# Kernel optimization log

Measured on AMD Instinct MI355X. Metric: run time of the kernel, lower is better.

The kernel has to match this reference:

```python
import jax, jax.numpy as jnp
import numpy as np

B, L, D, H, P = 8, 1024, 128, 128, 8
W = 2 * L  # total words
FT = 0.1   # forget-gate floor


def _lin_init(k, out_d, in_d):
    k1, k2 = jax.random.split(k)
    s = 1.0 / np.sqrt(in_d)
    Wm = jax.random.uniform(k1, (out_d, in_d), minval=-s, maxval=s, dtype=jnp.float32)
    b = jax.random.uniform(k2, (out_d,), minval=-s, maxval=s, dtype=jnp.float32)
    return Wm, b


def setup_inputs() -> dict:
    key = jax.random.key(0)
    ks = jax.random.split(key, 32)
    inp = {
        "word_span0": jax.random.normal(ks[0], (B, L, D), dtype=jnp.float32),
        "word_span1": jax.random.normal(ks[1], (B, L, D), dtype=jnp.float32),
        "node_hidden": jax.random.normal(ks[2], (B, D), dtype=jnp.float32),
        "op_embedding": jax.random.normal(ks[3], (B, P, D), dtype=jnp.float32),
        "word_exist_sequence": jax.random.uniform(ks[4], (B, W), dtype=jnp.float32),
        "word_exist_matrix": jax.random.uniform(ks[5], (B, W, W), dtype=jnp.float32),
        "word_operator": jax.random.uniform(ks[6], (B, W, P), dtype=jnp.float32),
        "word_word": jax.random.uniform(ks[7], (B, W, W), dtype=jnp.float32),
        "depend0": jax.random.uniform(ks[8], (B, L, L), dtype=jnp.float32),
        "depend1": jax.random.uniform(ks[9], (B, L, L), dtype=jnp.float32),
        "goal_word": jax.random.uniform(ks[10], (B, W), dtype=jnp.float32),
    }
    dims = [("w_w_s", H, D), ("w_w_k", H, D), ("w_update", D, 3 * H),
            ("g_w", H, D), ("w_o", D, D), ("b2u_forget", D, 3 * H + D),
            ("b2u_forget2", D, 2 * D), ("linear_output", D, D),
            ("o_w", H, D), ("w_g", D, D), ("u2b_forget", D, 2 * D),
            ("w_o_forget", P, D + P * D), ("w_o_rel", P, D + P * D),
            ("w_o_update", P, 2 * P)]
    for i, (nm, o, ii) in enumerate(dims):
        Wm, b = _lin_init(ks[11 + i], o, ii)
        inp[nm + "_W"] = Wm
        inp[nm + "_b"] = b
    return inp


def _lin(x, Wm, b):
    return x @ Wm.T + b


def _nrm(m):
    # row-normalize by count of nonzero entries (torch normalize_matrix)
    return m / ((m != 0).sum(-1, keepdims=True).astype(m.dtype) + 1e-30)


def _l2(x):
    return x / (jnp.linalg.norm(x, axis=-1, keepdims=True) + 1e-30)


def _hgcn(span0, span1, node_hidden, op_emb, wes, wem, w_op, ww, dep0, dep1, gw, p):
    # ---- Bottom2Up ----
    all_word = jnp.concatenate([span0, span1], axis=1)              # [B,W,D]
    goal_trans = _lin(node_hidden, p["g_w_W"], p["g_w_b"])[:, None, :]  # [B,1,H]
    word_g = _l2(goal_trans * gw[..., None])                        # [B,W,H]
    wk_trans = _lin(all_word, p["w_w_k_W"], p["w_w_k_b"])           # [B,W,H]
    word_w_k = _l2(_nrm(ww * wem) @ wk_trans)                       # [B,W,H]
    word_w_s = _l2(jnp.concatenate(
        [_nrm(dep0) @ _lin(span0, p["w_w_s_W"], p["w_w_s_b"]),
         _nrm(dep1) @ _lin(span1, p["w_w_s_W"], p["w_w_s_b"])], axis=1))
    neighbor = jnp.concatenate([word_g, word_w_k, word_w_s], axis=-1)  # [B,W,3H]
    forget = jax.nn.sigmoid(_lin(jnp.concatenate([all_word, word_g, word_w_k, word_w_s], axis=-1),
                                 p["b2u_forget_W"], p["b2u_forget_b"]))
    word_updated = jnp.clip(forget, FT) * all_word + (1 - forget) * jax.nn.relu(
        _lin(neighbor, p["w_update_W"], p["w_update_b"]))           # [B,W,D]
    word_op = _nrm(jnp.swapaxes(wes[..., None] * w_op, 1, 2)) @ _lin(
        word_updated, p["w_o_W"], p["w_o_b"])                       # [B,P,D]
    forget2 = jax.nn.sigmoid(_lin(jnp.concatenate([op_emb, word_op], axis=-1),
                                  p["b2u_forget2_W"], p["b2u_forget2_b"]))
    op_emb = jnp.clip(forget2, FT) * op_emb + (1 - forget2) * jax.nn.relu(
        _lin(word_op, p["linear_output_W"], p["linear_output_b"]))  # [B,P,D]

    # ---- update_graph ----
    awe_n = _l2(word_updated)
    op_n = _l2(op_emb).reshape(op_emb.shape[0], -1)                 # [B,P*D]
    concate = jnp.concatenate(
        [awe_n, jnp.broadcast_to(op_n[:, None, :], (awe_n.shape[0], awe_n.shape[1], op_n.shape[-1]))],
        axis=-1)                                                    # [B,W,D+P*D]
    fg = jnp.clip(jax.nn.sigmoid(_lin(concate, p["w_o_forget_W"], p["w_o_forget_b"])), FT)
    upd = jax.nn.softmax(jax.nn.relu(_lin(
        jnp.concatenate([w_op, _lin(concate, p["w_o_rel_W"], p["w_o_rel_b"])], axis=-1),
        p["w_o_update_W"], p["w_o_update_b"])), axis=-1)
    w_op_new = fg * w_op + (1 - fg) * upd                           # [B,W,P]

    # ---- Up2Bottom ----
    span0u, span1u = word_updated[:, :L], word_updated[:, L:]
    word_o = _l2(w_op_new @ _lin(op_emb, p["o_w_W"], p["o_w_b"]))   # [B,W,H]
    word_w_k2 = _l2(_nrm(ww * wem) @ _lin(word_updated, p["w_w_k_W"], p["w_w_k_b"]))
    word_w_s2 = _l2(jnp.concatenate(
        [_nrm(dep0) @ _lin(span0u, p["w_w_s_W"], p["w_w_s_b"]),
         _nrm(dep1) @ _lin(span1u, p["w_w_s_W"], p["w_w_s_b"])], axis=1))
    neighbor2 = jnp.concatenate([word_o, word_w_k2, word_w_s2], axis=-1)
    word_updated2 = jax.nn.relu(_lin(neighbor2, p["w_update_W"], p["w_update_b"]))  # [B,W,D]
    goal_w = jnp.einsum('bw,bwd->bd', _nrm(gw * wes), word_updated2)  # [B,D]
    goal_updated = jax.nn.relu(_lin(goal_w, p["w_g_W"], p["w_g_b"]))
    fg3 = jax.nn.sigmoid(_lin(jnp.concatenate([goal_w, node_hidden], axis=-1),
                              p["u2b_forget_W"], p["u2b_forget_b"]))
    goal_next = jnp.clip(fg3, FT) * node_hidden + (1 - fg3) * goal_updated
    return (span0u, span1u, op_emb, goal_next)


def reference(word_span0, word_span1, node_hidden, op_embedding, word_exist_sequence,
              word_exist_matrix, word_operator, word_word, depend0, depend1, goal_word,
              w_w_s_W, w_w_s_b, w_w_k_W, w_w_k_b, w_update_W, w_update_b,
              g_w_W, g_w_b, w_o_W, w_o_b, b2u_forget_W, b2u_forget_b,
              b2u_forget2_W, b2u_forget2_b, linear_output_W, linear_output_b,
              o_w_W, o_w_b, w_g_W, w_g_b, u2b_forget_W, u2b_forget_b,
              w_o_forget_W, w_o_forget_b, w_o_rel_W, w_o_rel_b, w_o_update_W, w_o_update_b):
    p = dict(w_w_s_W=w_w_s_W, w_w_s_b=w_w_s_b, w_w_k_W=w_w_k_W, w_w_k_b=w_w_k_b,
             w_update_W=w_update_W, w_update_b=w_update_b, g_w_W=g_w_W, g_w_b=g_w_b,
             w_o_W=w_o_W, w_o_b=w_o_b, b2u_forget_W=b2u_forget_W, b2u_forget_b=b2u_forget_b,
             b2u_forget2_W=b2u_forget2_W, b2u_forget2_b=b2u_forget2_b,
             linear_output_W=linear_output_W, linear_output_b=linear_output_b,
             o_w_W=o_w_W, o_w_b=o_w_b, w_g_W=w_g_W, w_g_b=w_g_b,
             u2b_forget_W=u2b_forget_W, u2b_forget_b=u2b_forget_b,
             w_o_forget_W=w_o_forget_W, w_o_forget_b=w_o_forget_b,
             w_o_rel_W=w_o_rel_W, w_o_rel_b=w_o_rel_b,
             w_o_update_W=w_o_update_W, w_o_update_b=w_o_update_b)
    return _hgcn(word_span0, word_span1, node_hidden, op_embedding, word_exist_sequence,
                 word_exist_matrix, word_operator, word_word, depend0, depend1, goal_word, p)
```

## Files before the change

### kernel.cpp

```cpp
#include <hip/hip_runtime.h>

constexpr int Bn = 8, Ln = 1024, Dn = 128, Pn = 8, Wn = 2048;
constexpr float FTc = 0.1f;
constexpr int BLDc = Bn * Ln * Dn;
constexpr int BWDc = Bn * Wn * Dn;
constexpr int IDM = 1 << 28;

struct __align__(16) F4 { float v[4]; };

typedef __attribute__((ext_vector_type(8))) __bf16 bf16x8;
typedef __attribute__((ext_vector_type(8))) short short8v;
typedef __attribute__((ext_vector_type(4))) short short4v;
typedef __attribute__((ext_vector_type(4))) float f32x4;

static __device__ __forceinline__ float sigm(float x) { return 1.f / (1.f + expf(-x)); }

static __device__ __forceinline__ short f2bf(float f) {
    unsigned u = __builtin_bit_cast(unsigned, f);
    unsigned r = (u + 0x7FFFu + ((u >> 16) & 1u)) >> 16;
    return (short)r;
}

template<int NSRC, int ACT, int OUT, int BM>
__global__ __launch_bounds__(256)
void linmfma(const short* __restrict__ x0, const short* __restrict__ x1,
             const short* __restrict__ x2, const short* __restrict__ x3,
             const float* __restrict__ Wt, const float* __restrict__ bias,
             float* __restrict__ Y, short* __restrict__ Yh, short* __restrict__ Xblk,
             int in_mod, int in_stride, int in_off,
             int out_mod, int out_stride, int out_off,
             const float* __restrict__ fbuf, const float* __restrict__ bbuf)
{
    constexpr int K = NSRC * 128;
    constexpr int NKB = K / 64;
    constexpr int WRr = BM / 16;
    constexpr int WC = 4 / WRr;
    constexpr int NF = 8 / WC;
    constexpr int CPW = 128 / WC;
    __shared__ short sX[BM * 72];
    __shared__ short sW[128 * 72];

    const int tid = threadIdx.x;
    const int wave = tid >> 6, lane = tid & 63;
    const int l15 = lane & 15, l4 = lane >> 4;
    const int rg = wave % WRr, cg = wave / WRr;
    const int n0 = blockIdx.x * BM;
    const int inRow0  = (n0 / in_mod)  * in_stride  + (n0 % in_mod)  + in_off;
    const int outRow0 = (n0 / out_mod) * out_stride + (n0 % out_mod) + out_off;

    f32x4 acc[NF];
    #pragma unroll
    for (int nf = 0; nf < NF; ++nf) acc[nf] = (f32x4){0.f, 0.f, 0.f, 0.f};

    const int xrow = tid >> 3, xk8 = (tid & 7) * 8;

    for (int kb = 0; kb < NKB; ++kb) {
        const int k0 = kb * 64;
        __syncthreads();
        if (tid < BM * 8) {
            const short* __restrict__ src;
            { int s = k0 >> 7; src = (s == 0) ? x0 : (s == 1) ? x1 : (s == 2) ? x2 : x3; }
            const int koff = k0 & 127;
            *(short8v*)&sX[xrow * 72 + xk8] =
                *(const short8v*)(src + (size_t)(inRow0 + xrow) * 128 + koff + xk8);
        }
        #pragma unroll
        for (int it = 0; it < 4; ++it) {
            int idx = tid + it * 256;
            int m = idx >> 3, k8 = (idx & 7) * 8;
            const float* pw = Wt + (size_t)m * K + k0 + k8;
            F4 v0 = *(const F4*)pw, v1 = *(const F4*)(pw + 4);
            short8v sv;
            #pragma unroll
            for (int e = 0; e < 4; ++e) { sv[e] = f2bf(v0.v[e]); sv[4 + e] = f2bf(v1.v[e]); }
            *(short8v*)&sW[m * 72 + k8] = sv;
        }
        __syncthreads();
        #pragma unroll
        for (int ksub = 0; ksub < 2; ++ksub) {
            bf16x8 af = *(const bf16x8*)&sX[(rg * 16 + l15) * 72 + ksub * 32 + l4 * 8];
            #pragma unroll
            for (int nf = 0; nf < NF; ++nf) {
                bf16x8 bv = *(const bf16x8*)&sW[(cg * CPW + nf * 16 + l15) * 72 + ksub * 32 + l4 * 8];
                acc[nf] = __builtin_amdgcn_mfma_f32_16x16x32_bf16(af, bv, acc[nf], 0, 0, 0);
            }
        }
    }

    const int r0 = rg * 16 + l4 * 4;
    float vals[NF][4];
    #pragma unroll
    for (int nf = 0; nf < NF; ++nf) {
        int col = cg * CPW + nf * 16 + l15;
        float bs = bias[col];
        #pragma unroll
        for (int r = 0; r < 4; ++r) {
            int row = outRow0 + r0 + r;
            float v = acc[nf][r] + bs;
            if constexpr (ACT == 1) v = fmaxf(v, 0.f);
            if constexpr (ACT == 2) v = sigm(v);
            if constexpr (ACT == 3) {
                float f = fbuf[(size_t)row * 128 + col];
                float base = bbuf[(size_t)row * 128 + col];
                v = fmaxf(f, FTc) * base + (1.f - f) * fmaxf(v, 0.f);
            }
            vals[nf][r] = v;
            if constexpr (OUT & 1) Y[(size_t)row * 128 + col] = v;
            if constexpr (OUT & 2) Yh[(size_t)row * 128 + col] = f2bf(v);
        }
    }
    if constexpr (OUT & 4) {
        short* sS = sW;
        __syncthreads();
        #pragma unroll
        for (int nf = 0; nf < NF; ++nf) {
            int col = cg * CPW + nf * 16 + l15;
            #pragma unroll
            for (int r = 0; r < 4; ++r)
                sS[col * 40 + r0 + r] = f2bf(vals[nf][r]);
        }
        __syncthreads();
        const int bb = outRow0 >> 11, kbo = (outRow0 & 2047) >> 5;
        short* __restrict__ dst = Xblk + ((size_t)(bb * 64 + kbo)) * 4096;
        #pragma unroll
        for (int it = 0; it < 2; ++it) {
            int t2 = tid + it * 256;
            int col = t2 >> 2, k8 = (t2 & 3) * 8;
            *(short8v*)(dst + (size_t)t2 * 8) = *(const short8v*)&sS[col * 40 + k8];
        }
    }
}

template<int AMODE, bool WRA>
__global__ __launch_bounds__(256)
void mfma_part(const float* __restrict__ A0, const float* __restrict__ A1,
               const short* __restrict__ Abf, short* __restrict__ Awr,
               const short* __restrict__ Xblk, float* __restrict__ part,
               int NI, int KJ, int KL, int xkb0)
{
    __shared__ short sA[32 * 72];
    __shared__ short sB[128 * 72];
    const int tid = threadIdx.x;
    const int wave = tid >> 6, lane = tid & 63;
    const int l15 = lane & 15, l4 = lane >> 4;
    const int rg = wave >> 1, cg = wave & 1;
    const int b = blockIdx.y, kc = blockIdx.z;
    const int i0 = blockIdx.x * 32;
    const size_t aBase = ((size_t)b * NI + i0) * KJ + (size_t)kc * KL;
    const int nkb = KL >> 6;
    const int cbase = b * 64 + xkb0 + ((kc * KL) >> 5);
    const int arow = tid >> 3, ak16 = (tid & 7) * 8, ak8 = (tid & 3) * 8;

    f32x4 acc[4];
    #pragma unroll
    for (int nf = 0; nf < 4; ++nf) acc[nf] = (f32x4){0.f, 0.f, 0.f, 0.f};

    short8v ra;
    F4 rav0, rav1, raw0, raw1;
    short8v rb0, rb1, rb2, rb3;

#define LOADA(KB)                                                              \
    {                                                                          \
        size_t aoff = aBase + (size_t)arow * KJ + (KB)*64 + ak16;              \
        if constexpr (AMODE == 2) {                                            \
            ra = *(const short8v*)(Abf + aoff);                                \
        } else {                                                               \
            rav0 = *(const F4*)(A0 + aoff); rav1 = *(const F4*)(A0 + aoff + 4);\
            if constexpr (AMODE == 1) {                                        \
                raw0 = *(const F4*)(A1 + aoff); raw1 = *(const F4*)(A1 + aoff + 4); \
            }                                                                  \
        }                                                                      \
    }
#define STOREA(KB)                                                             \
    {                                                                          \
        short8v sv;                                                            \
        if constexpr (AMODE == 2) { sv = ra; }                                 \
        else {                                                                 \
            _Pragma("unroll")                                                  \
            for (int e = 0; e < 4; ++e) {                                      \
                float f0 = rav0.v[e], f1 = rav1.v[e];                          \
                if constexpr (AMODE == 1) { f0 *= raw0.v[e]; f1 *= raw1.v[e]; }\
                sv[e] = f2bf(f0); sv[4 + e] = f2bf(f1);                        \
            }                                                                  \
        }                                                                      \
        *(short8v*)&sA[arow * 72 + ak16] = sv;                                 \
        if constexpr (WRA)                                                     \
            *(short8v*)(Awr + aBase + (size_t)arow * KJ + (KB)*64 + ak16) = sv;\
    }
#define LOADB(KB)                                                              \
    {                                                                          \
        const short* s0 = Xblk + ((size_t)(cbase + (KB)*2)) * 4096;            \
        rb0 = *(const short8v*)(s0 + (size_t)tid * 8);                         \
        rb1 = *(const short8v*)(s0 + (size_t)(tid + 256) * 8);                 \
        rb2 = *(const short8v*)(s0 + 4096 + (size_t)tid * 8);                  \
        rb3 = *(const short8v*)(s0 + 4096 + (size_t)(tid + 256) * 8);          \
    }
#define STOREB()                                                               \
    {                                                                          \
        int c0 = tid >> 2;            int c1 = (tid + 256) >> 2;               \
        *(short8v*)&sB[c0 * 72 + ak8]      = rb0;                              \
        *(short8v*)&sB[c1 * 72 + ak8]      = rb1;                              \
        *(short8v*)&sB[c0 * 72 + 32 + ak8] = rb2;                              \
        *(short8v*)&sB[c1 * 72 + 32 + ak8] = rb3;                              \
    }

    LOADA(0); LOADB(0);
    STOREA(0); STOREB();
    __syncthreads();

    for (int kb = 0; kb < nkb; ++kb) {
        const bool more = (kb + 1 < nkb);
        if (more) { LOADA(kb + 1); LOADB(kb + 1); }
        #pragma unroll
        for (int ksub = 0; ksub < 2; ++ksub) {
            bf16x8 af = *(const bf16x8*)&sA[(rg * 16 + l15) * 72 + ksub * 32 + l4 * 8];
            #pragma unroll
            for (int nf = 0; nf < 4; ++nf) {
                bf16x8 bv = *(const bf16x8*)&sB[(cg * 64 + nf * 16 + l15) * 72 + ksub * 32 + l4 * 8];
                acc[nf] = __builtin_amdgcn_mfma_f32_16x16x32_bf16(af, bv, acc[nf], 0, 0, 0);
            }
        }
        if (more) {
            __syncthreads();
            STOREA(kb + 1); STOREB();
            __syncthreads();
        }
    }
#undef LOADA
#undef STOREA
#undef LOADB
#undef STOREB

    const size_t pbase = (((size_t)kc * Bn + b) * NI + i0 + rg * 16 + l4 * 4) * 128 + cg * 64;
    #pragma unroll
    for (int nf = 0; nf < 4; ++nf)
        #pragma unroll
        for (int r = 0; r < 4; ++r)
            part[pbase + (size_t)r * 128 + nf * 16 + l15] = acc[nf][r];
}

__global__ void k_gemm_fin(const float* __restrict__ part, short* __restrict__ Yh,
                           int NI, int KCH, int ybs, int yoff)
{
    int row = blockIdx.x; int b = row / NI; int i = row - b * NI;
    int h = threadIdx.x;
    float s = 0.f;
    for (int kc = 0; kc < KCH; ++kc)
        s += part[(((size_t)kc * Bn + b) * NI + i) * 128 + h];
    __shared__ float red[128];
    red[h] = s * s; __syncthreads();
    for (int st = 64; st > 0; st >>= 1) { if (h < st) red[h] += red[h + st]; __syncthreads(); }
    Yh[(size_t)(b * ybs + yoff + i) * 128 + h] = f2bf(s / (sqrtf(red[0]) + 1e-30f));
}

__global__ void k_allword(const float* __restrict__ s0, const float* __restrict__ s1,
                          float* __restrict__ aw, short* __restrict__ awh)
{
    int i = blockIdx.x * 256 + threadIdx.x;
    int b = i / (Ln * Dn / 4);
    F4 v0 = ((const F4*)s0)[i];
    F4 v1 = ((const F4*)s1)[i];
    int d0 = i + b * (Ln * Dn / 4);
    int d1 = i + (b + 1) * (Ln * Dn / 4);
    ((F4*)aw)[d0] = v0;
    ((F4*)aw)[d1] = v1;
    short4v h0, h1;
    #pragma unroll
    for (int e = 0; e < 4; ++e) { h0[e] = f2bf(v0.v[e]); h1[e] = f2bf(v1.v[e]); }
    ((short4v*)awh)[d0] = h0;
    ((short4v*)awh)[d1] = h1;
}

__global__ void k_goalg(const float* __restrict__ node, const float* __restrict__ Wg,
                        const float* __restrict__ bg, float* __restrict__ gvec,
                        float* __restrict__ gnorm)
{
    int b = blockIdx.x, h = threadIdx.x;
    float s = bg[h];
    for (int k = 0; k < 128; ++k) s += node[b * 128 + k] * Wg[h * 128 + k];
    gvec[b * 128 + h] = s;
    __shared__ float red[128];
    red[h] = s * s; __syncthreads();
    for (int st = 64; st > 0; st >>= 1) { if (h < st) red[h] += red[h + st]; __syncthreads(); }
    if (h == 0) gnorm[b] = sqrtf(red[0]);
}

__global__ void k_wordg(const float* __restrict__ gvec, const float* __restrict__ gnorm,
                        const float* __restrict__ gw, short* __restrict__ wgh)
{
    int row = blockIdx.x; int b = row >> 11; int h = threadIdx.x;
    float s = gw[row];
    float coef = s / (s * gnorm[b] + 1e-30f);
    wgh[(size_t)row * 128 + h] = f2bf(gvec[b * 128 + h] * coef);
}

__global__ __launch_bounds__(256)
void k_wordop_part(const float* __restrict__ wes, const float* __restrict__ wopr,
                   const float* __restrict__ Yl, float* __restrict__ part,
                   float* __restrict__ pcnt)
{
    int c = blockIdx.x, b = blockIdx.y;
    int w0 = c * 32;
    __shared__ float sc[32][8];
    int tid = threadIdx.x;
    {
        int w = tid >> 3, p = tid & 7;
        sc[w][p] = wes[b * Wn + w0 + w] * wopr[(size_t)(b * Wn + w0 + w) * Pn + p];
    }
    __syncthreads();
    if (tid < 8) {
        float n = 0.f;
        for (int w = 0; w < 32; ++w) n += (sc[w][tid] != 0.f) ? 1.f : 0.f;
        pcnt[(c * 8 + b) * 8 + tid] = n;
    }
    int d = tid & 127, g = tid >> 7;
    float acc[4] = {};
    for (int w = 0; w < 32; ++w) {
        float y = Yl[(size_t)(b * Wn + w0 + w) * 128 + d];
        #pragma unroll
        for (int q = 0; q < 4; ++q) acc[q] += sc[w][g * 4 + q] * y;
    }
    #pragma unroll
    for (int q = 0; q < 4; ++q)
        part[(((size_t)c * 8 + b) * 8 + g * 4 + q) * 128 + d] = acc[q];
}

__global__ void k_wordop_fin(const float* __restrict__ part, const float* __restrict__ pcnt,
                             float* __restrict__ outp)
{
    int bp = blockIdx.x;
    int b = bp >> 3, p = bp & 7;
    int d = threadIdx.x;
    float s = 0.f, n = 0.f;
    for (int c = 0; c < 64; ++c) s += part[(((size_t)c * 8 + b) * 8 + p) * 128 + d];
    for (int c = 0; c < 64; ++c) n += pcnt[(c * 8 + b) * 8 + p];
    outp[(size_t)bp * 128 + d] = s / (n + 1e-30f);
}

__global__ void k_opemb(const float* __restrict__ oein, const float* __restrict__ wop,
                        const float* __restrict__ W2, const float* __restrict__ b2,
                        const float* __restrict__ Wlo, const float* __restrict__ blo,
                        float* __restrict__ opembN, float* __restrict__ out2)
{
    int bp = blockIdx.x; int h = threadIdx.x;
    const float* oe = oein + (size_t)bp * 128;
    const float* wo = wop + (size_t)bp * 128;
    float s = b2[h], lo = blo[h];
    for (int k = 0; k < 128; ++k) {
        s += oe[k] * W2[h * 256 + k];
        s += wo[k] * W2[h * 256 + 128 + k];
        lo += wo[k] * Wlo[h * 128 + k];
    }
    float f = sigm(s);
    float v = fmaxf(f, FTc) * oe[h] + (1.f - f) * fmaxf(lo, 0.f);
    opembN[bp * 128 + h] = v;
    out2[bp * 128 + h] = v;
}

__global__ void k_opn(const float* __restrict__ opembN, float* __restrict__ opn)
{
    __shared__ float red[128];
    int bp = blockIdx.x, h = threadIdx.x;
    float v = opembN[bp * 128 + h];
    red[h] = v * v; __syncthreads();
    for (int s = 64; s > 0; s >>= 1) { if (h < s) red[h] += red[h + s]; __syncthreads(); }
    opn[bp * 128 + h] = v / (sqrtf(red[0]) + 1e-30f);
}

__global__ void k_cfrel(const float* __restrict__ opn, const float* __restrict__ Wf,
                        const float* __restrict__ bf, const float* __restrict__ Wr,
                        const float* __restrict__ br, float* __restrict__ cf,
                        float* __restrict__ crel)
{
    int bp = blockIdx.x; int b = bp >> 3, p = bp & 7;
    int t = threadIdx.x;
    float sf = 0.f, sr = 0.f;
    for (int k = t; k < 1024; k += 256) {
        float o = opn[b * 1024 + k];
        sf += o * Wf[p * 1152 + 128 + k];
        sr += o * Wr[p * 1152 + 128 + k];
    }
    __shared__ float rf[256], rr[256];
    rf[t] = sf; rr[t] = sr; __syncthreads();
    for (int s = 128; s > 0; s >>= 1) {
        if (t < s) { rf[t] += rf[t + s]; rr[t] += rr[t + s]; }
        __syncthreads();
    }
    if (t == 0) { cf[bp] = rf[0] + bf[p]; crel[bp] = rr[0] + br[p]; }
}

__global__ __launch_bounds__(256)
void k_fgrel(const float* __restrict__ wupd, const float* __restrict__ Wf,
             const float* __restrict__ Wr, const float* __restrict__ cf,
             const float* __restrict__ crel, float* __restrict__ fgb,
             float* __restrict__ relb)
{
    __shared__ float sXr[32 * 132];
    __shared__ float sinv[32];
    int tid = threadIdx.x;
    int n0 = blockIdx.x * 32;
    for (int l = tid; l < 4096; l += 256) {
        int r = l >> 7, h = l & 127;
        sXr[r * 132 + h] = wupd[(size_t)(n0 + r) * 128 + h];
    }
    __syncthreads();
    if (tid < 32) {
        float s = 0.f;
        for (int h = 0; h < 128; ++h) { float v = sXr[tid * 132 + h]; s += v * v; }
        sinv[tid] = 1.f / (sqrtf(s) + 1e-30f);
    }
    __syncthreads();
    int r = tid >> 3, p = tid & 7;
    int n = n0 + r; int b = n >> 11;
    float af = 0.f, ar = 0.f, inv = sinv[r];
    for (int d = 0; d < 128; ++d) {
        float x = sXr[r * 132 + d] * inv;
        af += x * Wf[p * 1152 + d];
        ar += x * Wr[p * 1152 + d];
    }
    float f = sigm(af + cf[b * 8 + p]);
    fgb[(size_t)n * 8 + p] = fmaxf(f, FTc);
    relb[(size_t)n * 8 + p] = ar + crel[b * 8 + p];
}

__global__ void k_wopnew(const float* __restrict__ wopr, const float* __restrict__ fgb,
                         const float* __restrict__ relb, const float* __restrict__ Wu,
                         const float* __restrict__ bu, float* __restrict__ wopn)
{
    int row = blockIdx.x * 256 + threadIdx.x;
    float t16[16];
    #pragma unroll
    for (int p = 0; p < 8; ++p) t16[p] = wopr[(size_t)row * 8 + p];
    #pragma unroll
    for (int p = 0; p < 8; ++p) t16[8 + p] = relb[(size_t)row * 8 + p];
    float u[8]; float m = -1e30f;
    #pragma unroll
    for (int p = 0; p < 8; ++p) {
        float s = bu[p];
        #pragma unroll
        for (int q = 0; q < 16; ++q) s += Wu[p * 16 + q] * t16[q];
        s = fmaxf(s, 0.f); u[p] = s; m = fmaxf(m, s);
    }
    float tot = 0.f;
    #pragma unroll
    for (int p = 0; p < 8; ++p) { u[p] = expf(u[p] - m); tot += u[p]; }
    float itot = 1.f / tot;
    #pragma unroll
    for (int p = 0; p < 8; ++p) {
        float f = fgb[(size_t)row * 8 + p];
        wopn[(size_t)row * 8 + p] = f * t16[p] + (1.f - f) * u[p] * itot;
    }
}

__global__ void k_opw(const float* __restrict__ opembN, const float* __restrict__ Wo,
                      const float* __restrict__ bo, float* __restrict__ opw)
{
    int bp = blockIdx.x, h = threadIdx.x;
    float s = bo[h];
    for (int d = 0; d < 128; ++d) s += opembN[bp * 128 + d] * Wo[h * 128 + d];
    opw[bp * 128 + h] = s;
}

__global__ void k_wordo(const float* __restrict__ wopn, const float* __restrict__ opw,
                        short* __restrict__ woh)
{
    int row = blockIdx.x; int b = row >> 11; int h = threadIdx.x;
    float c[8];
    #pragma unroll
    for (int p = 0; p < 8; ++p) c[p] = wopn[(size_t)row * 8 + p];
    float v = 0.f;
    #pragma unroll
    for (int p = 0; p < 8; ++p) v += c[p] * opw[(b * 8 + p) * 128 + h];
    __shared__ float red[128];
    red[h] = v * v; __syncthreads();
    for (int s = 64; s > 0; s >>= 1) { if (h < s) red[h] += red[h + s]; __syncthreads(); }
    woh[(size_t)row * 128 + h] = f2bf(v / (sqrtf(red[0]) + 1e-30f));
}

__global__ __launch_bounds__(256)
void k_goalw_part(const float* __restrict__ gw, const float* __restrict__ wes,
                  const float* __restrict__ wupd2, float* __restrict__ part,
                  float* __restrict__ pcnt)
{
    int c = blockIdx.x, b = blockIdx.y;
    int w0 = c * 32;
    __shared__ float sc[32];
    __shared__ float sa[256];
    int tid = threadIdx.x;
    if (tid < 32) sc[tid] = gw[b * Wn + w0 + tid] * wes[b * Wn + w0 + tid];
    __syncthreads();
    if (tid == 0) {
        float n = 0.f;
        for (int w = 0; w < 32; ++w) n += (sc[w] != 0.f) ? 1.f : 0.f;
        pcnt[c * 8 + b] = n;
    }
    int d = tid & 127, h = tid >> 7;
    float acc = 0.f;
    for (int w = h; w < 32; w += 2)
        acc += sc[w] * wupd2[(size_t)(b * Wn + w0 + w) * 128 + d];
    sa[tid] = acc; __syncthreads();
    if (h == 0) part[((size_t)c * 8 + b) * 128 + d] = sa[d] + sa[128 + d];
}

__global__ void k_goalw_fin(const float* __restrict__ part, const float* __restrict__ pcnt,
                            float* __restrict__ goalw)
{
    int b = blockIdx.x, d = threadIdx.x;
    float s = 0.f, n = 0.f;
    for (int c = 0; c < 64; ++c) s += part[((size_t)c * 8 + b) * 128 + d];
    for (int c = 0; c < 64; ++c) n += pcnt[c * 8 + b];
    goalw[b * 128 + d] = s / (n + 1e-30f);
}

__global__ void k_goalnext(const float* __restrict__ goalw, const float* __restrict__ node,
                           const float* __restrict__ Wg, const float* __restrict__ bg,
                           const float* __restrict__ Wu2, const float* __restrict__ bu2,
                           float* __restrict__ outg)
{
    int b = blockIdx.x, h = threadIdx.x;
    float su = bg[h], sf = bu2[h];
    for (int k = 0; k < 128; ++k) {
        float g = goalw[b * 128 + k];
        su += g * Wg[h * 128 + k];
        sf += g * Wu2[h * 256 + k] + node[b * 128 + k] * Wu2[h * 256 + 128 + k];
    }
    float gu = fmaxf(su, 0.f);
    float f = sigm(sf);
    outg[b * 128 + h] = fmaxf(f, FTc) * node[b * 128 + h] + (1.f - f) * gu;
}

__global__ void k_copyspans(const float* __restrict__ wupd, float* __restrict__ out)
{
    int i = blockIdx.x * 256 + threadIdx.x;
    F4 v = ((const F4*)wupd)[i];
    int row = i >> 5;
    int col = i & 31;
    int b = row >> 11, w = row & 2047;
    int dst;
    if (w < Ln) dst = ((b * Ln + w) << 5) + col;
    else        dst = (BLDc >> 2) + ((b * Ln + (w - Ln)) << 5) + col;
    ((F4*)out)[dst] = v;
}

extern "C" void kernel_launch(void* const* d_in, const int* in_sizes, int n_in,
                              void* d_out, int out_size, void* d_ws, size_t ws_size,
                              hipStream_t stream)
{
    const float* span0 = (const float*)d_in[0];
    const float* span1 = (const float*)d_in[1];
    const float* node  = (const float*)d_in[2];
    const float* opemb = (const float*)d_in[3];
    const float* wes   = (const float*)d_in[4];
    const float* wem   = (const float*)d_in[5];
    const float* wopr  = (const float*)d_in[6];
    const float* ww    = (const float*)d_in[7];
    const float* dep0  = (const float*)d_in[8];
    const float* dep1  = (const float*)d_in[9];
    const float* gw    = (const float*)d_in[10];
    const float* wws_W = (const float*)d_in[11]; const float* wws_b = (const float*)d_in[12];
    const float* wwk_W = (const float*)d_in[13]; const float* wwk_b = (const float*)d_in[14];
    const float* wup_W = (const float*)d_in[15]; const float* wup_b = (const float*)d_in[16];
    const float* gw_W  = (const float*)d_in[17]; const float* gw_b  = (const float*)d_in[18];
    const float* wo_W  = (const float*)d_in[19]; const float* wo_b  = (const float*)d_in[20];
    const float* bf_W  = (const float*)d_in[21]; const float* bf_b  = (const float*)d_in[22];
    const float* bf2_W = (const float*)d_in[23]; const float* bf2_b = (const float*)d_in[24];
    const float* lo_W  = (const float*)d_in[25]; const float* lo_b  = (const float*)d_in[26];
    const float* ow_W  = (const float*)d_in[27]; const float* ow_b  = (const float*)d_in[28];
    const float* wg_W  = (const float*)d_in[29]; const float* wg_b  = (const float*)d_in[30];
    const float* u2b_W = (const float*)d_in[31]; const float* u2b_b = (const float*)d_in[32];
    const float* wof_W = (const float*)d_in[33]; const float* wof_b = (const float*)d_in[34];
    const float* wor_W = (const float*)d_in[35]; const float* wor_b = (const float*)d_in[36];
    const float* wou_W = (const float*)d_in[37]; const float* wou_b = (const float*)d_in[38];

    float* out = (float*)d_out;
    float* out_op   = out + 2 * BLDc;
    float* out_goal = out + 2 * BLDc + Bn * Pn * Dn;

    float* ws = (float*)d_ws;
    float* allword = ws;
    float* wupd    = ws + 1 * BWDc;
    float* tmpA    = ws + 2 * BWDc;
    float* tmpB    = ws + 3 * BWDc;
    float* sm      = ws + 4 * BWDc;
    float* gvec   = sm;
    float* gnorm  = sm + 1024;
    float* wordop = sm + 1056;
    float* opembN = sm + 9248;
    float* opn    = sm + 17440;
    float* cf     = sm + 25632;
    float* crel   = sm + 25696;
    float* opw    = sm + 25760;
    float* goalw  = sm + 33952;
    float* fgb    = sm + 34976;
    float* relb   = sm + 166048;
    float* wopn   = sm + 297120;

    short* allwordh = (short*)(ws + 4 * (size_t)BWDc + 458752);
    short* wupdh  = allwordh + BWDc;
    short* wordgh = wupdh + BWDc;
    short* wwkh   = wordgh + BWDc;
    short* wwsh   = wwkh + BWDc;
    short* Xblk   = wwsh + BWDc;
    short* Awwem  = Xblk + BWDc;
    short* dep0b  = Awwem + (size_t)Bn * Wn * Wn;
    short* dep1b  = dep0b + (size_t)Bn * Ln * Ln;

    float* partWW1 = (float*)dep0b;
    float* partWW2 = tmpA;
    float* partD0  = tmpA;
    float* partD1  = tmpB;

    const dim3 blk(256);

    k_allword<<<1024, blk, 0, stream>>>(span0, span1, allword, allwordh);
    linmfma<1,0,4,32><<<512, blk, 0, stream>>>(allwordh, nullptr, nullptr, nullptr,
        wwk_W, wwk_b, nullptr, nullptr, Xblk, IDM, 0, 0, IDM, 0, 0, nullptr, nullptr);
    mfma_part<1,true><<<dim3(64, 8, 4), blk, 0, stream>>>(ww, wem, nullptr, Awwem,
        Xblk, partWW1, Wn, Wn, 512, 0);
    k_gemm_fin<<<16384, 128, 0, stream>>>(partWW1, wwkh, Wn, 4, Wn, 0);
    linmfma<1,0,4,32><<<256, blk, 0, stream>>>(allwordh, nullptr, nullptr, nullptr,
        wws_W, wws_b, nullptr, nullptr, Xblk, Ln, Wn, 0, Ln, Wn, 0, nullptr, nullptr);
    linmfma<1,0,4,32><<<256, blk, 0, stream>>>(allwordh, nullptr, nullptr, nullptr,
        wws_W, wws_b, nullptr, nullptr, Xblk, Ln, Wn, Ln, Ln, Wn, Ln, nullptr, nullptr);
    mfma_part<0,true><<<dim3(32, 8, 2), blk, 0, stream>>>(dep0, nullptr, nullptr, dep0b,
        Xblk, partD0, Ln, Ln, 512, 0);
    k_gemm_fin<<<8192, 128, 0, stream>>>(partD0, wwsh, Ln, 2, Wn, 0);
    mfma_part<0,true><<<dim3(32, 8, 2), blk, 0, stream>>>(dep1, nullptr, nullptr, dep1b,
        Xblk, partD1, Ln, Ln, 512, 32);
    k_gemm_fin<<<8192, 128, 0, stream>>>(partD1, wwsh, Ln, 2, Wn, Ln);
    k_goalg<<<8, 128, 0, stream>>>(node, gw_W, gw_b, gvec, gnorm);
    k_wordg<<<16384, 128, 0, stream>>>(gvec, gnorm, gw, wordgh);
    linmfma<4,2,1,16><<<1024, blk, 0, stream>>>(allwordh, wordgh, wwkh, wwsh,
        bf_W, bf_b, tmpB, nullptr, nullptr, IDM, 0, 0, IDM, 0, 0, nullptr, nullptr);
    linmfma<3,3,3,16><<<1024, blk, 0, stream>>>(wordgh, wwkh, wwsh, nullptr,
        wup_W, wup_b, wupd, wupdh, nullptr, IDM, 0, 0, IDM, 0, 0, tmpB, allword);
    linmfma<1,0,1,16><<<1024, blk, 0, stream>>>(wupdh, nullptr, nullptr, nullptr,
        wo_W, wo_b, tmpA, nullptr, nullptr, IDM, 0, 0, IDM, 0, 0, nullptr, nullptr);
    k_wordop_part<<<dim3(64, 8), blk, 0, stream>>>(wes, wopr, tmpA, tmpB, tmpB + 524288);
    k_wordop_fin<<<64, 128, 0, stream>>>(tmpB, tmpB + 524288, wordop);
    k_opemb<<<64, 128, 0, stream>>>(opemb, wordop, bf2_W, bf2_b, lo_W, lo_b, opembN, out_op);
    k_opn<<<64, 128, 0, stream>>>(opembN, opn);
    k_cfrel<<<64, blk, 0, stream>>>(opn, wof_W, wof_b, wor_W, wor_b, cf, crel);
    k_fgrel<<<512, blk, 0, stream>>>(wupd, wof_W, wor_W, cf, crel, fgb, relb);
    k_wopnew<<<64, blk, 0, stream>>>(wopr, fgb, relb, wou_W, wou_b, wopn);
    k_opw<<<64, 128, 0, stream>>>(opembN, ow_W, ow_b, opw);
    k_wordo<<<16384, 128, 0, stream>>>(wopn, opw, wordgh);

    linmfma<1,0,4,32><<<512, blk, 0, stream>>>(wupdh, nullptr, nullptr, nullptr,
        wwk_W, wwk_b, nullptr, nullptr, Xblk, IDM, 0, 0, IDM, 0, 0, nullptr, nullptr);
    mfma_part<2,false><<<dim3(64, 8, 2), blk, 0, stream>>>(nullptr, nullptr, Awwem, nullptr,
        Xblk, partWW2, Wn, Wn, 1024, 0);
    k_gemm_fin<<<16384, 128, 0, stream>>>(partWW2, wwkh, Wn, 2, Wn, 0);
    linmfma<1,0,4,32><<<256, blk, 0, stream>>>(wupdh, nullptr, nullptr, nullptr,
        wws_W, wws_b, nullptr, nullptr, Xblk, Ln, Wn, 0, Ln, Wn, 0, nullptr, nullptr);
    linmfma<1,0,4,32><<<256, blk, 0, stream>>>(wupdh, nullptr, nullptr, nullptr,
        wws_W, wws_b, nullptr, nullptr, Xblk, Ln, Wn, Ln, Ln, Wn, Ln, nullptr, nullptr);
    mfma_part<2,false><<<dim3(32, 8, 2), blk, 0, stream>>>(nullptr, nullptr, dep0b, nullptr,
        Xblk, partD0, Ln, Ln, 512, 0);
    k_gemm_fin<<<8192, 128, 0, stream>>>(partD0, wwsh, Ln, 2, Wn, 0);
    mfma_part<2,false><<<dim3(32, 8, 2), blk, 0, stream>>>(nullptr, nullptr, dep1b, nullptr,
        Xblk, partD1, Ln, Ln, 512, 32);
    k_gemm_fin<<<8192, 128, 0, stream>>>(partD1, wwsh, Ln, 2, Wn, Ln);
    linmfma<3,1,1,16><<<1024, blk, 0, stream>>>(wordgh, wwkh, wwsh, nullptr,
        wup_W, wup_b, tmpA, nullptr, nullptr, IDM, 0, 0, IDM, 0, 0, nullptr, nullptr);
    k_goalw_part<<<dim3(64, 8), blk, 0, stream>>>(gw, wes, tmpA, tmpB, tmpB + 65536);
    k_goalw_fin<<<8, 128, 0, stream>>>(tmpB, tmpB + 65536, goalw);
    k_goalnext<<<8, 128, 0, stream>>>(goalw, node, wg_W, wg_b, u2b_W, u2b_b, out_goal);
    k_copyspans<<<2048, blk, 0, stream>>>(wupd, out);
}
```

Before: 410.4 us.

## Fuse wwk/wws projections, enlarge GEMM tiles, store split-K partials in bf16

Adds a lin2x kernel that computes the w_w_k and w_w_s projections from a single load of the input rows into separate blocked buffers, replacing three linmfma launches per round with one. The adjacency GEMM kernel now uses 64-row tiles with each wave covering all 128 columns, and the split-K partition is changed (2 chunks for word_word, 4 for the dependency matrices). Split-K partial sums are written as bf16 instead of fp32 and reduced by a new finisher, which halves partial-sum traffic at some cost in accuracy. Scratch buffers are reassigned so the two projection outputs can coexist.

Result: faster. 376.7 us (-8.2%).

```diff
diff --git a/kernel.cpp b/kernel.cpp
--- a/kernel.cpp
+++ b/kernel.cpp
@@ -20,13 +20,16 @@
     unsigned r = (u + 0x7FFFu + ((u >> 16) & 1u)) >> 16;
     return (short)r;
 }
+static __device__ __forceinline__ float bf2f(short s) {
+    return __builtin_bit_cast(float, ((unsigned)(unsigned short)s) << 16);
+}
 
 template<int NSRC, int ACT, int OUT, int BM>
 __global__ __launch_bounds__(256)
 void linmfma(const short* __restrict__ x0, const short* __restrict__ x1,
              const short* __restrict__ x2, const short* __restrict__ x3,
              const float* __restrict__ Wt, const float* __restrict__ bias,
-             float* __restrict__ Y, short* __restrict__ Yh, short* __restrict__ Xblk,
+             float* __restrict__ Y, short* __restrict__ Yh,
              int in_mod, int in_stride, int in_off,
              int out_mod, int out_stride, int out_off,
              const float* __restrict__ fbuf, const float* __restrict__ bbuf)
@@ -88,7 +91,6 @@
     }
 
     const int r0 = rg * 16 + l4 * 4;
-    float vals[NF][4];
     #pragma unroll
     for (int nf = 0; nf < NF; ++nf) {
         int col = cg * CPW + nf * 16 + l15;
@@ -104,88 +106,166 @@
                 float base = bbuf[(size_t)row * 128 + col];
                 v = fmaxf(f, FTc) * base + (1.f - f) * fmaxf(v, 0.f);
             }
-            vals[nf][r] = v;
             if constexpr (OUT & 1) Y[(size_t)row * 128 + col] = v;
             if constexpr (OUT & 2) Yh[(size_t)row * 128 + col] = f2bf(v);
         }
     }
-    if constexpr (OUT & 4) {
-        short* sS = sW;
+}
+
+__global__ __launch_bounds__(256)
+void lin2x(const short* __restrict__ x0,
+           const float* __restrict__ W0, const float* __restrict__ b0v,
+           const float* __restrict__ W1, const float* __restrict__ b1v,
+           short* __restrict__ Xout0, short* __restrict__ Xout1)
+{
+    __shared__ short sX[32 * 72];
+    __shared__ short sW[2][128 * 72];
+    const int tid = threadIdx.x;
+    const int wave = tid >> 6, lane = tid & 63;
+    const int l15 = lane & 15, l4 = lane >> 4;
+    const int rg = wave & 1, cg = wave >> 1;
+    const int n0 = blockIdx.x * 32;
+
+    f32x4 acc[2][4];
+    #pragma unroll
+    for (int o = 0; o < 2; ++o) {
+        #pragma unroll
+        for (int nf = 0; nf < 4; ++nf) {
+            acc[o][nf] = (f32x4){0.f, 0.f, 0.f, 0.f};
+        }
+    }
+
+    const int xrow = tid >> 3, xk8 = (tid & 7) * 8;
+
+    #pragma unroll
+    for (int kb = 0; kb < 2; ++kb) {
+        const int k0 = kb * 64;
         __syncthreads();
-        #pragma unroll
-        for (int nf = 0; nf < NF; ++nf) {
-            int col = cg * CPW + nf * 16 + l15;
+        *(short8v*)&sX[xrow * 72 + xk8] =
+            *(const short8v*)(x0 + (size_t)(n0 + xrow) * 128 + k0 + xk8);
+        #pragma unroll
+        for (int o = 0; o < 2; ++o) {
+            const float* __restrict__ Wt = o ? W1 : W0;
             #pragma unroll
-            for (int r = 0; r < 4; ++r)
-                sS[col * 40 + r0 + r] = f2bf(vals[nf][r]);
+            for (int it = 0; it < 4; ++it) {
+                int idx = tid + it * 256;
+                int m = idx >> 3, k8 = (idx & 7) * 8;
+                const float* pw = Wt + (size_t)m * 128 + k0 + k8;
+                F4 v0 = *(const F4*)pw, v1 = *(const F4*)(pw + 4);
+                short8v sv;
+                #pragma unroll
+                for (int e = 0; e < 4; ++e) { sv[e] = f2bf(v0.v[e]); sv[4 + e] = f2bf(v1.v[e]); }
+                *(short8v*)&sW[o][m * 72 + k8] = sv;
+            }
         }
         __syncthreads();
-        const int bb = outRow0 >> 11, kbo = (outRow0 & 2047) >> 5;
-        short* __restrict__ dst = Xblk + ((size_t)(bb * 64 + kbo)) * 4096;
+        #pragma unroll
+        for (int ksub = 0; ksub < 2; ++ksub) {
+            bf16x8 af = *(const bf16x8*)&sX[(rg * 16 + l15) * 72 + ksub * 32 + l4 * 8];
+            #pragma unroll
+            for (int o = 0; o < 2; ++o) {
+                #pragma unroll
+                for (int nf = 0; nf < 4; ++nf) {
+                    bf16x8 bv = *(const bf16x8*)&sW[o][(cg * 64 + nf * 16 + l15) * 72 + ksub * 32 + l4 * 8];
+                    acc[o][nf] = __builtin_amdgcn_mfma_f32_16x16x32_bf16(af, bv, acc[o][nf], 0, 0, 0);
+                }
+            }
+        }
+    }
+
+    const int r0 = rg * 16 + l4 * 4;
+    __syncthreads();
+    #pragma unroll
+    for (int o = 0; o < 2; ++o) {
+        const float* bv = o ? b1v : b0v;
+        #pragma unroll
+        for (int nf = 0; nf < 4; ++nf) {
+            int col = cg * 64 + nf * 16 + l15;
+            float bs = bv[col];
+            #pragma unroll
+            for (int r = 0; r < 4; ++r) {
+                sW[o][col * 40 + r0 + r] = f2bf(acc[o][nf][r] + bs);
+            }
+        }
+    }
+    __syncthreads();
+    const int bb = n0 >> 11, kbo = (n0 & 2047) >> 5;
+    #pragma unroll
+    for (int o = 0; o < 2; ++o) {
+        short* __restrict__ dst = (o ? Xout1 : Xout0) + ((size_t)(bb * 64 + kbo)) * 4096;
         #pragma unroll
         for (int it = 0; it < 2; ++it) {
             int t2 = tid + it * 256;
             int col = t2 >> 2, k8 = (t2 & 3) * 8;
-            *(short8v*)(dst + (size_t)t2 * 8) = *(const short8v*)&sS[col * 40 + k8];
+            *(short8v*)(dst + (size_t)t2 * 8) = *(const short8v*)&sW[o][col * 40 + k8];
         }
     }
 }
 
 template<int AMODE, bool WRA>
 __global__ __launch_bounds__(256)
-void mfma_part(const float* __restrict__ A0, const float* __restrict__ A1,
-               const short* __restrict__ Abf, short* __restrict__ Awr,
-               const short* __restrict__ Xblk, float* __restrict__ part,
-               int NI, int KJ, int KL, int xkb0)
-{
-    __shared__ short sA[32 * 72];
+void mfma_gemm5(const float* __restrict__ A0, const float* __restrict__ A1,
+                const short* __restrict__ Abf, short* __restrict__ Awr,
+                const short* __restrict__ Xblk, short* __restrict__ part,
+                int NI, int KJ, int KL, int xkb0)
+{
+    __shared__ short sA[64 * 72];
     __shared__ short sB[128 * 72];
     const int tid = threadIdx.x;
     const int wave = tid >> 6, lane = tid & 63;
     const int l15 = lane & 15, l4 = lane >> 4;
-    const int rg = wave >> 1, cg = wave & 1;
     const int b = blockIdx.y, kc = blockIdx.z;
-    const int i0 = blockIdx.x * 32;
+    const int i0 = blockIdx.x * 64;
     const size_t aBase = ((size_t)b * NI + i0) * KJ + (size_t)kc * KL;
     const int nkb = KL >> 6;
     const int cbase = b * 64 + xkb0 + ((kc * KL) >> 5);
-    const int arow = tid >> 3, ak16 = (tid & 7) * 8, ak8 = (tid & 3) * 8;
-
-    f32x4 acc[4];
-    #pragma unroll
-    for (int nf = 0; nf < 4; ++nf) acc[nf] = (f32x4){0.f, 0.f, 0.f, 0.f};
-
-    short8v ra;
-    F4 rav0, rav1, raw0, raw1;
+    const int arow = tid >> 2, ak = (tid & 3) * 16;
+    const int bk8 = (tid & 3) * 8;
+
+    f32x4 acc[8];
+    #pragma unroll
+    for (int nf = 0; nf < 8; ++nf) acc[nf] = (f32x4){0.f, 0.f, 0.f, 0.f};
+
+    short8v ra0, ra1;
+    F4 rav0, rav1, rav2, rav3, raw0, raw1, raw2, raw3;
     short8v rb0, rb1, rb2, rb3;
 
 #define LOADA(KB)                                                              \
     {                                                                          \
-        size_t aoff = aBase + (size_t)arow * KJ + (KB)*64 + ak16;              \
+        size_t aoff = aBase + (size_t)arow * KJ + (KB)*64 + ak;                \
         if constexpr (AMODE == 2) {                                            \
-            ra = *(const short8v*)(Abf + aoff);                                \
+            ra0 = *(const short8v*)(Abf + aoff);                               \
+            ra1 = *(const short8v*)(Abf + aoff + 8);                           \
         } else {                                                               \
-            rav0 = *(const F4*)(A0 + aoff); rav1 = *(const F4*)(A0 + aoff + 4);\
+            rav0 = *(const F4*)(A0 + aoff);      rav1 = *(const F4*)(A0 + aoff + 4); \
+            rav2 = *(const F4*)(A0 + aoff + 8);  rav3 = *(const F4*)(A0 + aoff + 12);\
             if constexpr (AMODE == 1) {                                        \
-                raw0 = *(const F4*)(A1 + aoff); raw1 = *(const F4*)(A1 + aoff + 4); \
+                raw0 = *(const F4*)(A1 + aoff);      raw1 = *(const F4*)(A1 + aoff + 4); \
+                raw2 = *(const F4*)(A1 + aoff + 8);  raw3 = *(const F4*)(A1 + aoff + 12);\
             }                                                                  \
         }                                                                      \
     }
 #define STOREA(KB)                                                             \
     {                                                                          \
-        short8v sv;                                                            \
-        if constexpr (AMODE == 2) { sv = ra; }                                 \
+        short8v sv0, sv1;                                                      \
+        if constexpr (AMODE == 2) { sv0 = ra0; sv1 = ra1; }                    \
         else {                                                                 \
             _Pragma("unroll")                                                  \
             for (int e = 0; e < 4; ++e) {                                      \
-                float f0 = rav0.v[e], f1 = rav1.v[e];                          \
-                if constexpr (AMODE == 1) { f0 *= raw0.v[e]; f1 *= raw1.v[e]; }\
-                sv[e] = f2bf(f0); sv[4 + e] = f2bf(f1);                        \
+                float a0 = rav0.v[e], a1 = rav1.v[e], a2 = rav2.v[e], a3 = rav3.v[e]; \
+                if constexpr (AMODE == 1) { a0 *= raw0.v[e]; a1 *= raw1.v[e];  \
+                                            a2 *= raw2.v[e]; a3 *= raw3.v[e]; }\
+                sv0[e] = f2bf(a0); sv0[4 + e] = f2bf(a1);                      \
+                sv1[e] = f2bf(a2); sv1[4 + e] = f2bf(a3);                      \
             }                                                                  \
         }                                                                      \
-        *(short8v*)&sA[arow * 72 + ak16] = sv;                                 \
-        if constexpr (WRA)                                                     \
-            *(short8v*)(Awr + aBase + (size_t)arow * KJ + (KB)*64 + ak16) = sv;\
+        *(short8v*)&sA[arow * 72 + ak]     = sv0;                              \
+        *(short8v*)&sA[arow * 72 + ak + 8] = sv1;                              \
+        if constexpr (WRA) {                                                   \
+            size_t aoff = aBase + (size_t)arow * KJ + (KB)*64 + ak;            \
+            *(short8v*)(Awr + aoff)     = sv0;                                 \
+            *(short8v*)(Awr + aoff + 8) = sv1;                                 \
+        }                                                                      \
     }
 #define LOADB(KB)                                                              \
     {                                                                          \
@@ -198,10 +278,10 @@
 #define STOREB()                                                               \
     {                                                                          \
         int c0 = tid >> 2;            int c1 = (tid + 256) >> 2;               \
-        *(short8v*)&sB[c0 * 72 + ak8]      = rb0;                              \
-        *(short8v*)&sB[c1 * 72 + ak8]      = rb1;                              \
-        *(short8v*)&sB[c0 * 72 + 32 + ak8] = rb2;                              \
-        *(short8v*)&sB[c1 * 72 + 32 + ak8] = rb3;                              \
+        *(short8v*)&sB[c0 * 72 + bk8]      = rb0;                              \
+        *(short8v*)&sB[c1 * 72 + bk8]      = rb1;                              \
+        *(short8v*)&sB[c0 * 72 + 32 + bk8] = rb2;                              \
+        *(short8v*)&sB[c1 * 72 + 32 + bk8] = rb3;                              \
     }
 
     LOADA(0); LOADB(0);
@@ -213,10 +293,10 @@
         if (more) { LOADA(kb + 1); LOADB(kb + 1); }
         #pragma unroll
         for (int ksub = 0; ksub < 2; ++ksub) {
-            bf16x8 af = *(const bf16x8*)&sA[(rg * 16 + l15) * 72 + ksub * 32 + l4 * 8];
+            bf16x8 af = *(const bf16x8*)&sA[(wave * 16 + l15) * 72 + ksub * 32 + l4 * 8];
             #pragma unroll
-            for (int nf = 0; nf < 4; ++nf) {
-                bf16x8 bv = *(const bf16x8*)&sB[(cg * 64 + nf * 16 + l15) * 72 + ksub * 32 + l4 * 8];
+            for (int nf = 0; nf < 8; ++nf) {
+                bf16x8 bv = *(const bf16x8*)&sB[(nf * 16 + l15) * 72 + ksub * 32 + l4 * 8];
                 acc[nf] = __builtin_amdgcn_mfma_f32_16x16x32_bf16(af, bv, acc[nf], 0, 0, 0);
             }
         }
@@ -231,22 +311,24 @@
 #undef LOADB
 #undef STOREB
 
-    const size_t pbase = (((size_t)kc * Bn + b) * NI + i0 + rg * 16 + l4 * 4) * 128 + cg * 64;
-    #pragma unroll
-    for (int nf = 0; nf < 4; ++nf)
-        #pragma unroll
-        for (int r = 0; r < 4; ++r)
-            part[pbase + (size_t)r * 128 + nf * 16 + l15] = acc[nf][r];
-}
-
-__global__ void k_gemm_fin(const float* __restrict__ part, short* __restrict__ Yh,
-                           int NI, int KCH, int ybs, int yoff)
+    const size_t pbase = (((size_t)kc * Bn + b) * NI + i0 + wave * 16 + l4 * 4) * 128;
+    #pragma unroll
+    for (int nf = 0; nf < 8; ++nf) {
+        #pragma unroll
+        for (int r = 0; r < 4; ++r) {
+            part[pbase + (size_t)r * 128 + nf * 16 + l15] = f2bf(acc[nf][r]);
+        }
+    }
+}
+
+__global__ void k_gemm_finh(const short* __restrict__ part, short* __restrict__ Yh,
+                            int NI, int KCH, int ybs, int yoff)
 {
     int row = blockIdx.x; int b = row / NI; int i = row - b * NI;
     int h = threadIdx.x;
     float s = 0.f;
     for (int kc = 0; kc < KCH; ++kc)
-        s += part[(((size_t)kc * Bn + b) * NI + i) * 128 + h];
+        s += bf2f(part[(((size_t)kc * Bn + b) * NI + i) * 128 + h]);
     __shared__ float red[128];
     red[h] = s * s; __syncthreads();
     for (int st = 64; st > 0; st >>= 1) { if (h < st) red[h] += red[h + st]; __syncthreads(); }
@@ -605,37 +687,34 @@
     short* dep0b  = Awwem + (size_t)Bn * Wn * Wn;
     short* dep1b  = dep0b + (size_t)Bn * Ln * Ln;
 
-    float* partWW1 = (float*)dep0b;
-    float* partWW2 = tmpA;
-    float* partD0  = tmpA;
-    float* partD1  = tmpB;
+    short* XblkS1 = (short*)tmpA;
+    short* pWW1   = dep0b;
+    short* pDep1  = (short*)tmpB;
+    short* XblkS2 = (short*)allword;
+    short* pWW2   = (short*)tmpA;
+    short* pDep2  = (short*)tmpB;
 
     const dim3 blk(256);
 
     k_allword<<<1024, blk, 0, stream>>>(span0, span1, allword, allwordh);
-    linmfma<1,0,4,32><<<512, blk, 0, stream>>>(allwordh, nullptr, nullptr, nullptr,
-        wwk_W, wwk_b, nullptr, nullptr, Xblk, IDM, 0, 0, IDM, 0, 0, nullptr, nullptr);
-    mfma_part<1,true><<<dim3(64, 8, 4), blk, 0, stream>>>(ww, wem, nullptr, Awwem,
-        Xblk, partWW1, Wn, Wn, 512, 0);
-    k_gemm_fin<<<16384, 128, 0, stream>>>(partWW1, wwkh, Wn, 4, Wn, 0);
-    linmfma<1,0,4,32><<<256, blk, 0, stream>>>(allwordh, nullptr, nullptr, nullptr,
-        wws_W, wws_b, nullptr, nullptr, Xblk, Ln, Wn, 0, Ln, Wn, 0, nullptr, nullptr);
-    linmfma<1,0,4,32><<<256, blk, 0, stream>>>(allwordh, nullptr, nullptr, nullptr,
-        wws_W, wws_b, nullptr, nullptr, Xblk, Ln, Wn, Ln, Ln, Wn, Ln, nullptr, nullptr);
-    mfma_part<0,true><<<dim3(32, 8, 2), blk, 0, stream>>>(dep0, nullptr, nullptr, dep0b,
-        Xblk, partD0, Ln, Ln, 512, 0);
-    k_gemm_fin<<<8192, 128, 0, stream>>>(partD0, wwsh, Ln, 2, Wn, 0);
-    mfma_part<0,true><<<dim3(32, 8, 2), blk, 0, stream>>>(dep1, nullptr, nullptr, dep1b,
-        Xblk, partD1, Ln, Ln, 512, 32);
-    k_gemm_fin<<<8192, 128, 0, stream>>>(partD1, wwsh, Ln, 2, Wn, Ln);
+    lin2x<<<512, blk, 0, stream>>>(allwordh, wwk_W, wwk_b, wws_W, wws_b, Xblk, XblkS1);
+    mfma_gemm5<1,true><<<dim3(32, 8, 2), blk, 0, stream>>>(ww, wem, nullptr, Awwem,
+        Xblk, pWW1, Wn, Wn, 1024, 0);
+    k_gemm_finh<<<16384, 128, 0, stream>>>(pWW1, wwkh, Wn, 2, Wn, 0);
+    mfma_gemm5<0,true><<<dim3(16, 8, 4), blk, 0, stream>>>(dep0, nullptr, nullptr, dep0b,
+        XblkS1, pDep1, Ln, Ln, 256, 0);
+    k_gemm_finh<<<8192, 128, 0, stream>>>(pDep1, wwsh, Ln, 4, Wn, 0);
+    mfma_gemm5<0,true><<<dim3(16, 8, 4), blk, 0, stream>>>(dep1, nullptr, nullptr, dep1b,
+        XblkS1, pDep1, Ln, Ln, 256, 32);
+    k_gemm_finh<<<8192, 128, 0, stream>>>(pDep1, wwsh, Ln, 4, Wn, Ln);
     k_goalg<<<8, 128, 0, stream>>>(node, gw_W, gw_b, gvec, gnorm);
     k_wordg<<<16384, 128, 0, stream>>>(gvec, gnorm, gw, wordgh);
     linmfma<4,2,1,16><<<1024, blk, 0, stream>>>(allwordh, wordgh, wwkh, wwsh,
-        bf_W, bf_b, tmpB, nullptr, nullptr, IDM, 0, 0, IDM, 0, 0, nullptr, nullptr);
+        bf_W, bf_b, tmpB, nullptr, IDM, 0, 0, IDM, 0, 0, nullptr, nullptr);
     linmfma<3,3,3,16><<<1024, blk, 0, stream>>>(wordgh, wwkh, wwsh, nullptr,
-        wup_W, wup_b, wupd, wupdh, nullptr, IDM, 0, 0, IDM, 0, 0, tmpB, allword);
+        wup_W, wup_b, wupd, wupdh, IDM, 0, 0, IDM, 0, 0, tmpB, allword);
     linmfma<1,0,1,16><<<1024, blk, 0, stream>>>(wupdh, nullptr, nullptr, nullptr,
-        wo_W, wo_b, tmpA, nullptr, nullptr, IDM, 0, 0, IDM, 0, 0, nullptr, nullptr);
+        wo_W, wo_b, tmpA, nullptr, IDM, 0, 0, IDM, 0, 0, nullptr, nullptr);
     k_wordop_part<<<dim3(64, 8), blk, 0, stream>>>(wes, wopr, tmpA, tmpB, tmpB + 524288);
     k_wordop_fin<<<64, 128, 0, stream>>>(tmpB, tmpB + 524288, wordop);
     k_opemb<<<64, 128, 0, stream>>>(opemb, wordop, bf2_W, bf2_b, lo_W, lo_b, opembN, out_op);
@@ -646,23 +725,18 @@
     k_opw<<<64, 128, 0, stream>>>(opembN, ow_W, ow_b, opw);
     k_wordo<<<16384, 128, 0, stream>>>(wopn, opw, wordgh);
 
-    linmfma<1,0,4,32><<<512, blk, 0, stream>>>(wupdh, nullptr, nullptr, nullptr,
-        wwk_W, wwk_b, nullptr, nullptr, Xblk, IDM, 0, 0, IDM, 0, 0, nullptr, nullptr);
-    mfma_part<2,false><<<dim3(64, 8, 2), blk, 0, stream>>>(nullptr, nullptr, Awwem, nullptr,
-        Xblk, partWW2, Wn, Wn, 1024, 0);
-    k_gemm_fin<<<16384, 128, 0, stream>>>(partWW2, wwkh, Wn, 2, Wn, 0);
-    linmfma<1,0,4,32><<<256, blk, 0, stream>>>(wupdh, nullptr, nullptr, nullptr,
-        wws_W, wws_b, nullptr, nullptr, Xblk, Ln, Wn, 0, Ln, Wn, 0, nullptr, nullptr);
-    linmfma<1,0,4,32><<<256, blk, 0, stream>>>(wupdh, nullptr, nullptr, nullptr,
-        wws_W, wws_b, nullptr, nullptr, Xblk, Ln, Wn, Ln, Ln, Wn, Ln, nullptr, nullptr);
-    mfma_part<2,false><<<dim3(32, 8, 2), blk, 0, stream>>>(nullptr, nullptr, dep0b, nullptr,
-        Xblk, partD0, Ln, Ln, 512, 0);
-    k_gemm_fin<<<8192, 128, 0, stream>>>(partD0, wwsh, Ln, 2, Wn, 0);
-    mfma_part<2,false><<<dim3(32, 8, 2), blk, 0, stream>>>(nullptr, nullptr, dep1b, nullptr,
-        Xblk, partD1, Ln, Ln, 512, 32);
-    k_gemm_fin<<<8192, 128, 0, stream>>>(partD1, wwsh, Ln, 2, Wn, Ln);
+    lin2x<<<512, blk, 0, stream>>>(wupdh, wwk_W, wwk_b, wws_W, wws_b, Xblk, XblkS2);
+    mfma_gemm5<2,false><<<dim3(32, 8, 2), blk, 0, stream>>>(nullptr, nullptr, Awwem, nullptr,
+        Xblk, pWW2, Wn, Wn, 1024, 0);
+    k_gemm_finh<<<16384, 128, 0, stream>>>(pWW2, wwkh, Wn, 2, Wn, 0);
+    mfma_gemm5<2,false><<<dim3(16, 8, 4), blk, 0, stream>>>(nullptr, nullptr, dep0b, nullptr,
+        XblkS2, pDep2, Ln, Ln, 256, 0);
+    k_gemm_finh<<<8192, 128, 0, stream>>>(pDep2, wwsh, Ln, 4, Wn, 0);
+    mfma_gemm5<2,false><<<dim3(16, 8, 4), blk, 0, stream>>>(nullptr, nullptr, dep1b, nullptr,
+        XblkS2, pDep2, Ln, Ln, 256, 32);
+    k_gemm_finh<<<8192, 128, 0, stream>>>(pDep2, wwsh, Ln, 4, Wn, Ln);
     linmfma<3,1,1,16><<<1024, blk, 0, stream>>>(wordgh, wwkh, wwsh, nullptr,
-        wup_W, wup_b, tmpA, nullptr, nullptr, IDM, 0, 0, IDM, 0, 0, nullptr, nullptr);
+        wup_W, wup_b, tmpA, nullptr, IDM, 0, 0, IDM, 0, 0, nullptr, nullptr);
     k_goalw_part<<<dim3(64, 8), blk, 0, stream>>>(gw, wes, tmpA, tmpB, tmpB + 65536);
     k_goalw_fin<<<8, 128, 0, stream>>>(tmpB, tmpB + 65536, goalw);
     k_goalnext<<<8, 128, 0, stream>>>(goalw, node, wg_W, wg_b, u2b_W, u2b_b, out_goal);
```
